# Kernel tuning notes

Hardware: AMD Instinct MI355X
Metric: run time of the kernel (lower is better)

The kernel has to match this reference:

```python
import jax, jax.numpy as jnp
import numpy as np
from jax import lax

# Model config (matches init_kwargs)
D = 256          # input_size
DO = 256         # output_size
H = 512          # hidden_size
E = 8            # num_experts
NB = 4           # num_bands
R = 8            # lora_rank
ALPHA = 16.0     # lora_alpha
CAP_F = 1.25     # capacity_factor
F = 64           # dct_freq_features
N = 65536        # num tokens
CAP = int(CAP_F * N / E)  # 10240 tokens per expert (expert-choice capacity)


def setup_inputs() -> dict:
    key = jax.random.key(0)
    ks = jax.random.split(key, 14)
    s = 0.02
    return {
        "x": jax.random.normal(ks[0], (N, D), jnp.float32),
        "band": jax.random.randint(ks[1], (N,), 0, NB, jnp.int32),
        "W_dct": jax.random.normal(ks[2], (D, F), jnp.float32) * s,
        "W_gate": jax.random.normal(ks[3], (D + F, E), jnp.float32) * s,
        "W1": jax.random.normal(ks[4], (E, D + 1, H), jnp.float32) * s,
        "b1": jnp.zeros((E, H), jnp.float32),
        "A1": jax.random.normal(ks[5], (E, NB, D + 1, R), jnp.float32) * s,
        "B1": jax.random.normal(ks[6], (E, NB, R, H), jnp.float32) * s,
        "W2": jax.random.normal(ks[7], (E, H, DO), jnp.float32) * s,
        "b2": jnp.zeros((E, DO), jnp.float32),
        "A2": jax.random.normal(ks[8], (E, NB, H, R), jnp.float32) * s,
        "B2": jax.random.normal(ks[9], (E, NB, R, DO), jnp.float32) * s,
    }


def reference(x, band, W_dct, W_gate, W1, b1, A1, B1, W2, b2, A2, B2):
    scale = ALPHA / R
    # 1) Frequency-aware gating: concat spatial + (linear) DCT-like features.
    freq = x @ W_dct                                   # [N,F]
    logits = jnp.concatenate([x, freq], -1) @ W_gate   # [N,E]
    # Expert-choice: softmax over the TOKEN axis, each expert picks top-CAP tokens.
    scores = jax.nn.softmax(logits, axis=0)            # [N,E]
    g, idx = lax.top_k(scores.T, CAP)                  # [E,CAP] weights / token ids
    # 2) Dispatch: gather tokens (band scalar appended -> input_size+1 features).
    band_f = band.astype(x.dtype)[:, None] / NB        # [N,1]
    x_full = jnp.concatenate([x, band_f], -1)          # [N,D+1]
    xe = x_full[idx]                                   # [E,CAP,D+1]
    oh = jax.nn.one_hot(band[idx], NB, dtype=x.dtype)  # [E,CAP,NB]
    ohn = jnp.transpose(oh, (0, 2, 1))[..., None]      # [E,NB,CAP,1]
    # 3) Per-expert shared MLP with per-band LoRA adapters (layer 1).
    h = jnp.einsum('ecd,edh->ech', xe, W1) + b1[:, None, :]
    u = jnp.einsum('ecd,endr->encr', xe, A1) * ohn     # band-select low-rank code
    h = h + scale * jnp.einsum('encr,enrh->ech', u, B1)
    h = jax.nn.gelu(h)
    # Layer 2.
    o = jnp.einsum('ech,eho->eco', h, W2) + b2[:, None, :]
    v = jnp.einsum('ech,enhr->encr', h, A2) * ohn
    o = o + scale * jnp.einsum('encr,enro->eco', v, B2)
    # 4) Combine: scatter-add gate-weighted expert outputs (unselected tokens -> 0).
    y = jnp.zeros((N, DO), x.dtype)
    y = y.at[idx.reshape(-1)].add((g[..., None] * o).reshape(-1, DO))
    return y
```

## Files before the change

kernel.cpp:

```cpp
#include <hip/hip_runtime.h>
#include <hip/hip_bf16.h>
#include <math.h>

#define NTOK 65536
#define DIN 256
#define DOUT 256
#define HID 512
#define NEXP 8
#define NBAND 4
#define RANK 8
#define CAP 10240
#define NTILE 64
#define TILES_PER_E (CAP / NTILE)

#define W1CAT_PER_E (34 * 9 * 512)
#define B1CAT_OFF   (NEXP * W1CAT_PER_E)
#define B1CAT_PER_E (32 * 512)
#define W2CAT_OFF   (B1CAT_OFF + NEXP * B1CAT_PER_E)
#define W2CAT_PER_E (18 * 16 * 512)
#define B2CAT_OFF   (W2CAT_OFF + NEXP * W2CAT_PER_E)
#define B2CAT_PER_E (16 * 512)
#define PK_TOTAL    (B2CAT_OFF + NEXP * B2CAT_PER_E)
#define PK_F32_OFF  1200000

typedef short s16x8 __attribute__((ext_vector_type(8)));
typedef float f32x4 __attribute__((ext_vector_type(4)));

__device__ __forceinline__ unsigned key_of(float f) {
    unsigned u = __float_as_uint(f);
    return (u & 0x80000000u) ? ~u : (u | 0x80000000u);
}
__device__ __forceinline__ float gelu_fast(float v) {
    const float c = 0.7978845608028654f;
    float z = c * (v + 0.044715f * v * v * v);
    float e = __expf(2.0f * z);
    return v * (1.0f - __builtin_amdgcn_rcpf(e + 1.0f));
}
__device__ __forceinline__ ushort f2bf(float f) {
    unsigned u = __float_as_uint(f);
    return (ushort)((u + 0x7FFFu + ((u >> 16) & 1u)) >> 16);
}

__global__ __launch_bounds__(256) void k_logits(const float* __restrict__ x,
                                                const float* __restrict__ Wdct,
                                                const float* __restrict__ Wgate,
                                                float* __restrict__ logitsT,
                                                float* __restrict__ partials,
                                                float* __restrict__ y) {
    __shared__ float wefft[8][257];
    __shared__ float pr[4][8];
    int tid = threadIdx.x, w = tid >> 6, lane = tid & 63;

    {
        int d = tid;
        float acc[8];
#pragma unroll
        for (int e = 0; e < 8; ++e) acc[e] = Wgate[d * 8 + e];
        for (int f = 0; f < 64; ++f) {
            float wv = Wdct[d * 64 + f];
#pragma unroll
            for (int e = 0; e < 8; ++e) acc[e] += wv * Wgate[(256 + f) * 8 + e];
        }
#pragma unroll
        for (int e = 0; e < 8; ++e) wefft[e][d] = acc[e];
    }

    {
        float4 z = {0.f, 0.f, 0.f, 0.f};
        float4* yp = (float4*)(y + (size_t)blockIdx.x * 64 * DOUT);
        for (int i = tid; i < 4096; i += 256) yp[i] = z;
    }
    __syncthreads();

    float wje[4][8];
#pragma unroll
    for (int j = 0; j < 4; ++j)
#pragma unroll
        for (int e = 0; e < 8; ++e) wje[j][e] = wefft[e][lane * 4 + j];

    int wid = blockIdx.x * 4 + w;
    int nbase = wid * 16;
    float es = 0.f;
    for (int t = 0; t < 16; ++t) {
        int n = nbase + t;
        float4 v = *(const float4*)(x + (size_t)n * DIN + lane * 4);
        float acc[8];
#pragma unroll
        for (int e = 0; e < 8; ++e) acc[e] = 0.f;
#pragma unroll
        for (int j = 0; j < 4; ++j) {
            float vj = (j == 0) ? v.x : (j == 1) ? v.y : (j == 2) ? v.z : v.w;
#pragma unroll
            for (int e = 0; e < 8; ++e) acc[e] += vj * wje[j][e];
        }
#pragma unroll
        for (int off = 1; off < 64; off <<= 1) {
#pragma unroll
            for (int e = 0; e < 8; ++e) acc[e] += __shfl_xor(acc[e], off);
        }
        float out = acc[0];
#pragma unroll
        for (int e = 1; e < 8; ++e) if (lane == e) out = acc[e];
        if (lane < 8) {
            logitsT[(size_t)lane * NTOK + n] = out;
            es += expf(out);
        }
    }
    if (lane < 8) pr[w][lane] = es;
    __syncthreads();
    if (tid < 8) partials[(size_t)tid * 1024 + blockIdx.x] =
        pr[0][tid] + pr[1][tid] + pr[2][tid] + pr[3][tid];
}

__global__ __launch_bounds__(1024) void k_misc(const float* __restrict__ logitsT,
                                               const float* __restrict__ partials,
                                               float* __restrict__ colsum,
                                               int* __restrict__ idxbuf,
                                               const float* __restrict__ W1,
                                               const float* __restrict__ A1,
                                               const float* __restrict__ B1,
                                               const float* __restrict__ W2,
                                               const float* __restrict__ A2,
                                               const float* __restrict__ B2,
                                               ushort* __restrict__ pk) {
    if (blockIdx.x >= 8) {
        int id = (blockIdx.x - 8) * 1024 + threadIdx.x;
        if (id >= PK_TOTAL) return;
        float val;
        if (id < B1CAT_OFF) {
            int e = id / W1CAT_PER_E, rem = id % W1CAT_PER_E;
            int t = rem / (9 * 512); rem %= 9 * 512;
            int s = rem / 512; int q = rem & 511;
            int l = q >> 3, j = q & 7;
            int k = s * 32 + ((l >> 4) << 3) + j;
            int col = t * 16 + (l & 15);
            if (k > 256) val = 0.f;
            else if (col < 512) val = W1[((size_t)e * 257 + k) * 512 + col];
            else {
                int cu = col - 512;
                val = A1[(((size_t)e * NBAND + (cu >> 3)) * 257 + k) * RANK + (cu & 7)];
            }
        } else if (id < W2CAT_OFF) {
            int id2 = id - B1CAT_OFF;
            int e = id2 / B1CAT_PER_E, rem = id2 % B1CAT_PER_E;
            int t = rem / 512; int q = rem & 511;
            int l = q >> 3, j = q & 7;
            int k32 = ((l >> 4) << 3) + j;
            int col = t * 16 + (l & 15);
            val = 2.0f * B1[(((size_t)e * NBAND + (k32 >> 3)) * RANK + (k32 & 7)) * 512 + col];
        } else if (id < B2CAT_OFF) {
            int id2 = id - W2CAT_OFF;
            int e = id2 / W2CAT_PER_E, rem = id2 % W2CAT_PER_E;
            int t = rem / (16 * 512); rem %= 16 * 512;
            int s = rem / 512; int q = rem & 511;
            int l = q >> 3, j = q & 7;
            int k = s * 32 + ((l >> 4) << 3) + j;
            int col = t * 16 + (l & 15);
            if (col < 256) val = W2[((size_t)e * 512 + k) * 256 + col];
            else {
                int cv = col - 256;
                val = A2[(((size_t)e * NBAND + (cv >> 3)) * 512 + k) * RANK + (cv & 7)];
            }
        } else {
            int id2 = id - B2CAT_OFF;
            int e = id2 / B2CAT_PER_E, rem = id2 % B2CAT_PER_E;
            int t = rem / 512; int q = rem & 511;
            int l = q >> 3, j = q & 7;
            int k32 = ((l >> 4) << 3) + j;
            int col = t * 16 + (l & 15);
            val = 2.0f * B2[(((size_t)e * NBAND + (k32 >> 3)) * RANK + (k32 & 7)) * 256 + col];
        }
        pk[id] = f2bf(val);
        return;
    }
    __shared__ unsigned subh[16][257];
    __shared__ unsigned bins[256];
    __shared__ float ssum[16];
    __shared__ unsigned sval[2];
    __shared__ unsigned scnt, stcnt;
    __shared__ int ties_l[2048];
    int e = blockIdx.x, tid = threadIdx.x, w = tid >> 6, lane = tid & 63;
    const float* lp = logitsT + (size_t)e * NTOK;

    {
        float s = partials[(size_t)e * 1024 + tid];
#pragma unroll
        for (int off = 32; off > 0; off >>= 1) s += __shfl_xor(s, off);
        if (lane == 0) ssum[w] = s;
        __syncthreads();
        if (tid == 0) {
            float t = 0.f;
#pragma unroll
            for (int i = 0; i < 16; ++i) t += ssum[i];
            colsum[e] = t;
        }
    }

    unsigned pref = 0, rem = CAP;
    for (int p = 0; p < 4; ++p) {
        int shift = 24 - 8 * p;
        for (int i = tid; i < 16 * 257; i += 1024) ((unsigned*)subh)[i] = 0;
        __syncthreads();
        for (int it = 0; it < 64; ++it) {
            int n = it * 1024 + tid;
            unsigned k = key_of(lp[n]);
            bool ok = (p == 0) || ((k >> (shift + 8)) == pref);
            if (ok) atomicAdd(&subh[w][(k >> shift) & 255u], 1u);
        }
        __syncthreads();
        if (tid < 256) {
            unsigned c = 0;
#pragma unroll
            for (int ww = 0; ww < 16; ++ww) c += subh[ww][tid];
            bins[tid] = c;
        }
        __syncthreads();
        for (int off = 1; off < 256; off <<= 1) {
            unsigned add = (tid < 256 && tid + off < 256) ? bins[tid + off] : 0u;
            __syncthreads();
            if (tid < 256) bins[tid] += add;
            __syncthreads();
        }
        if (tid < 256) {
            unsigned snext = (tid == 255) ? 0u : bins[tid + 1];
            if (bins[tid] >= rem && snext < rem) {
                sval[0] = (pref << 8) | (unsigned)tid;
                sval[1] = rem - snext;
            }
        }
        __syncthreads();
        pref = sval[0];
        rem = sval[1];
        __syncthreads();
    }

    if (tid == 0) { scnt = 0; stcnt = 0; }
    __syncthreads();
    unsigned T = pref;
    for (int it = 0; it < 64; ++it) {
        int n = it * 1024 + tid;
        unsigned k = key_of(lp[n]);
        if (k > T) {
            unsigned pos = atomicAdd(&scnt, 1u);
            idxbuf[e * CAP + pos] = n;
        } else if (k == T) {
            unsigned tp = atomicAdd(&stcnt, 1u);
            if (tp < 2048) ties_l[tp] = n;
        }
    }
    __syncthreads();
    int m = (int)stcnt, r = (int)rem, base = CAP - r;
    if (m == r) {
        for (int i = tid; i < m; i += 1024) idxbuf[e * CAP + base + i] = ties_l[i];
    } else {
        for (int i = tid; i < m; i += 1024) {
            int my = ties_l[i];
            int rank = 0;
            for (int j = 0; j < m; ++j) rank += (ties_l[j] < my);
            if (rank < r) idxbuf[e * CAP + base + rank] = my;
        }
    }
}

__global__ __launch_bounds__(256, 2) void k_expert(
    const float* __restrict__ x, const int* __restrict__ band,
    const float* __restrict__ b1, const float* __restrict__ b2,
    const ushort* __restrict__ pk,
    const float* __restrict__ logitsT,
    const float* __restrict__ colsum, const int* __restrict__ idxbuf,
    float* __restrict__ y) {
    __shared__ ushort bW1[9216];
    __shared__ ushort bW2[9216];
    __shared__ ushort sc[4][640];
    __shared__ int s_tok[4][16];
    __shared__ int s_band[4][16];
    __shared__ float s_g[4][16];

    int tid = threadIdx.x, w = tid >> 6, lane = tid & 63;
    int bid = blockIdx.x;
    int e = bid & 7;
    int tile = bid >> 3;

    if (lane < 16) {
        int n = idxbuf[e * CAP + tile * NTILE + w * 16 + lane];
        s_tok[w][lane] = n;
        s_band[w][lane] = band[n];
        s_g[w][lane] = expf(logitsT[(size_t)e * NTOK + n]) / colsum[e];
    }

    int l15 = lane & 15, lg = lane >> 4;
    ushort* scw = &sc[w][0];

    s16x8 a1[9];
    {
        int mytok = s_tok[w][l15];
        const float* xrow = x + (size_t)mytok * DIN;
        int kg = lg << 3;
#pragma unroll
        for (int s = 0; s < 8; ++s) {
            float4 p = *(const float4*)&xrow[s * 32 + kg];
            float4 q = *(const float4*)&xrow[s * 32 + kg + 4];
            s16x8 a;
            a[0] = (short)f2bf(p.x); a[1] = (short)f2bf(p.y);
            a[2] = (short)f2bf(p.z); a[3] = (short)f2bf(p.w);
            a[4] = (short)f2bf(q.x); a[5] = (short)f2bf(q.y);
            a[6] = (short)f2bf(q.z); a[7] = (short)f2bf(q.w);
            a1[s] = a;
        }
        s16x8 a = (s16x8)(short)0;
        if (lane < 16) a[0] = (short)f2bf((float)s_band[w][l15] * 0.25f);
        a1[8] = a;
    }

    const ushort* w1base = pk + (size_t)e * W1CAT_PER_E;
    const ushort* b1base = pk + B1CAT_OFF + (size_t)e * B1CAT_PER_E;
    const ushort* w2base = pk + W2CAT_OFF + (size_t)e * W2CAT_PER_E;
    const ushort* b2base = pk + B2CAT_OFF + (size_t)e * B2CAT_PER_E;

    s16x8 stg[9];
    if (w < 2) {
        const ushort* s0 = w2base + (size_t)(w * 9) * 16 * 512 + lane * 8;
#pragma unroll
        for (int i = 0; i < 9; ++i)
            stg[i] = *(const s16x8*)(s0 + (size_t)i * 16 * 512);
    } else {
        const ushort* s0 = w1base + (size_t)(w - 2) * 9 * 512 + lane * 8;
#pragma unroll
        for (int i = 0; i < 9; ++i)
            stg[i] = *(const s16x8*)(s0 + i * 512);
    }

    s16x8 ufrag;
    {
#pragma unroll
        for (int t = 32; t <= 33; ++t) {
            f32x4 acc = {0.f, 0.f, 0.f, 0.f};
#pragma unroll
            for (int s = 0; s < 9; ++s) {
                s16x8 b = *(const s16x8*)(w1base + ((size_t)t * 9 + s) * 512 + lane * 8);
                acc = __builtin_amdgcn_mfma_f32_16x16x32_bf16(a1[s], b, acc, 0, 0, 0);
            }
            int colbase = (t - 32) * 16 + l15;
#pragma unroll
            for (int r = 0; r < 4; ++r) {
                int row = lg * 4 + r;
                float v = ((colbase >> 3) == s_band[w][row]) ? acc[r] : 0.f;
                scw[row * 40 + colbase] = f2bf(v);
            }
        }
        ufrag = *(const s16x8*)&scw[l15 * 40 + lg * 8];
    }

    f32x4 oacc[16];
#pragma unroll
    for (int t2 = 0; t2 < 16; ++t2) {
        float bv = b2[(size_t)e * DOUT + t2 * 16 + l15];
        oacc[t2] = (f32x4){bv, bv, bv, bv};
    }
    f32x4 vacc[2];
    vacc[0] = (f32x4){0.f, 0.f, 0.f, 0.f};
    vacc[1] = (f32x4){0.f, 0.f, 0.f, 0.f};

    if (w < 2) {
#pragma unroll
        for (int i = 0; i < 9; ++i)
            *(s16x8*)(&bW2[(w * 9 + i) * 512] + lane * 8) = stg[i];
    } else {
#pragma unroll
        for (int i = 0; i < 9; ++i)
            *(s16x8*)(&bW1[((w - 2) * 9 + i) * 512] + lane * 8) = stg[i];
    }
    __syncthreads();

#pragma unroll 1
    for (int p = 0; p < 16; ++p) {
        s16x8 st2[9];
        if (p < 15) {
            int p1 = p + 1;
            if (w < 2) {
                const ushort* s0 = w2base + ((size_t)(w * 9) * 16 + p1) * 512 + lane * 8;
#pragma unroll
                for (int i = 0; i < 9; ++i)
                    st2[i] = *(const s16x8*)(s0 + (size_t)i * 16 * 512);
            } else {
                int t = p1 * 2 + (w - 2);
                const ushort* s0 = w1base + (size_t)t * 9 * 512 + lane * 8;
#pragma unroll
                for (int i = 0; i < 9; ++i)
                    st2[i] = *(const s16x8*)(s0 + i * 512);
            }
        }
#pragma unroll
        for (int half = 0; half < 2; ++half) {
            int t = p * 2 + half;
            float bv = b1[(size_t)e * HID + t * 16 + l15];
            f32x4 acc = {bv, bv, bv, bv};
#pragma unroll
            for (int s = 0; s < 9; ++s) {
                s16x8 b = *(const s16x8*)(&bW1[(half * 9 + s) * 512] + lane * 8);
                acc = __builtin_amdgcn_mfma_f32_16x16x32_bf16(a1[s], b, acc, 0, 0, 0);
            }
            {
                s16x8 b = *(const s16x8*)(b1base + (size_t)t * 512 + lane * 8);
                acc = __builtin_amdgcn_mfma_f32_16x16x32_bf16(ufrag, b, acc, 0, 0, 0);
            }
#pragma unroll
            for (int r = 0; r < 4; ++r) {
                int row = lg * 4 + r;
                scw[row * 40 + half * 16 + l15] = f2bf(gelu_fast(acc[r]));
            }
        }
        s16x8 hfrag = *(const s16x8*)&scw[l15 * 40 + lg * 8];
#pragma unroll
        for (int t2 = 0; t2 < 16; ++t2) {
            s16x8 b = *(const s16x8*)(&bW2[t2 * 512] + lane * 8);
            oacc[t2] = __builtin_amdgcn_mfma_f32_16x16x32_bf16(hfrag, b, oacc[t2], 0, 0, 0);
        }
#pragma unroll
        for (int i = 0; i < 2; ++i) {
            s16x8 b = *(const s16x8*)(&bW2[(16 + i) * 512] + lane * 8);
            vacc[i] = __builtin_amdgcn_mfma_f32_16x16x32_bf16(hfrag, b, vacc[i], 0, 0, 0);
        }
        if (p < 15) {
            __syncthreads();
            if (w < 2) {
#pragma unroll
                for (int i = 0; i < 9; ++i)
                    *(s16x8*)(&bW2[(w * 9 + i) * 512] + lane * 8) = st2[i];
            } else {
#pragma unroll
                for (int i = 0; i < 9; ++i)
                    *(s16x8*)(&bW1[((w - 2) * 9 + i) * 512] + lane * 8) = st2[i];
            }
            __syncthreads();
        }
    }

    s16x8 vfrag;
    {
#pragma unroll
        for (int i = 0; i < 2; ++i) {
            int colbase = i * 16 + l15;
#pragma unroll
            for (int r = 0; r < 4; ++r) {
                int row = lg * 4 + r;
                float v = ((colbase >> 3) == s_band[w][row]) ? vacc[i][r] : 0.f;
                scw[row * 40 + colbase] = f2bf(v);
            }
        }
        vfrag = *(const s16x8*)&scw[l15 * 40 + lg * 8];
    }

    float g4[4];
    int tok4[4];
#pragma unroll
    for (int r = 0; r < 4; ++r) {
        int row = lg * 4 + r;
        g4[r] = s_g[w][row];
        tok4[r] = s_tok[w][row];
    }
#pragma unroll
    for (int t2 = 0; t2 < 16; ++t2) {
        s16x8 b = *(const s16x8*)(b2base + (size_t)t2 * 512 + lane * 8);
        f32x4 acc = __builtin_amdgcn_mfma_f32_16x16x32_bf16(vfrag, b, oacc[t2], 0, 0, 0);
        int col = t2 * 16 + l15;
#pragma unroll
        for (int r = 0; r < 4; ++r) {
            atomicAdd(&y[(size_t)tok4[r] * DOUT + col], g4[r] * acc[r]);
        }
    }
}

extern "C" void kernel_launch(void* const* d_in, const int* in_sizes, int n_in,
                              void* d_out, int out_size, void* d_ws, size_t ws_size,
                              hipStream_t stream) {
    const float* x = (const float*)d_in[0];
    const int* band = (const int*)d_in[1];
    const float* Wdct = (const float*)d_in[2];
    const float* Wgate = (const float*)d_in[3];
    const float* W1 = (const float*)d_in[4];
    const float* b1 = (const float*)d_in[5];
    const float* A1 = (const float*)d_in[6];
    const float* B1 = (const float*)d_in[7];
    const float* W2 = (const float*)d_in[8];
    const float* b2 = (const float*)d_in[9];
    const float* A2 = (const float*)d_in[10];
    const float* B2 = (const float*)d_in[11];
    float* y = (float*)d_out;

    float* ws = (float*)d_ws;
    float* logitsT = ws;
    float* partials = ws + 524288;
    float* colsum = ws + 532480;
    int* idxbuf = (int*)(ws + 532488);
    ushort* pk = (ushort*)(ws + PK_F32_OFF);

    k_logits<<<1024, 256, 0, stream>>>(x, Wdct, Wgate, logitsT, partials, y);
    k_misc<<<8 + PK_TOTAL / 1024, 1024, 0, stream>>>(logitsT, partials, colsum,
                                                     idxbuf, W1, A1, B1, W2, A2,
                                                     B2, pk);
    k_expert<<<NEXP * TILES_PER_E, 256, 0, stream>>>(x, band, b1, b2, pk,
                                                     logitsT, colsum, idxbuf, y);
}
```

Measured before the change: 287.7 us.

## Build 16-bit key histogram in logits kernel to replace 4-pass radix top-k select

The logits kernel now atomically bins the top 16 bits of each logit's sortable key into a per-expert global histogram. The selection kernel uses that histogram in one prefix-scan pass to find the threshold bin, replacing four radix-histogram passes over all 65536 logits per expert. Ties within the threshold bin are written to a global buffer and ranked by full key then index, which can be quadratic if that bin is large. The expert kernel's launch bound also moves from 2 to 3 blocks per SIMD, which may cause register spilling.

```diff
diff --git a/kernel.cpp b/kernel.cpp
--- a/kernel.cpp
+++ b/kernel.cpp
@@ -12,6 +12,7 @@
 #define CAP 10240
 #define NTILE 64
 #define TILES_PER_E (CAP / NTILE)
+#define TIEMAX 7000
 
 #define W1CAT_PER_E (34 * 9 * 512)
 #define B1CAT_OFF   (NEXP * W1CAT_PER_E)
@@ -46,7 +47,8 @@
                                                 const float* __restrict__ Wgate,
                                                 float* __restrict__ logitsT,
                                                 float* __restrict__ partials,
-                                                float* __restrict__ y) {
+                                                float* __restrict__ y,
+                                                unsigned* __restrict__ hist16) {
     __shared__ float wefft[8][257];
     __shared__ float pr[4][8];
     int tid = threadIdx.x, w = tid >> 6, lane = tid & 63;
@@ -104,6 +106,7 @@
         if (lane < 8) {
             logitsT[(size_t)lane * NTOK + n] = out;
             es += expf(out);
+            atomicAdd(&hist16[((size_t)lane << 16) + (key_of(out) >> 16)], 1u);
         }
     }
     if (lane < 8) pr[w][lane] = es;
@@ -116,6 +119,8 @@
                                                const float* __restrict__ partials,
                                                float* __restrict__ colsum,
                                                int* __restrict__ idxbuf,
+                                               const unsigned* __restrict__ hist16,
+                                               int* __restrict__ tbuf,
                                                const float* __restrict__ W1,
                                                const float* __restrict__ A1,
                                                const float* __restrict__ B1,
@@ -173,14 +178,14 @@
         pk[id] = f2bf(val);
         return;
     }
-    __shared__ unsigned subh[16][257];
-    __shared__ unsigned bins[256];
+    __shared__ unsigned chunk[1024];
     __shared__ float ssum[16];
     __shared__ unsigned sval[2];
     __shared__ unsigned scnt, stcnt;
-    __shared__ int ties_l[2048];
     int e = blockIdx.x, tid = threadIdx.x, w = tid >> 6, lane = tid & 63;
     const float* lp = logitsT + (size_t)e * NTOK;
+    const unsigned* h = hist16 + ((size_t)e << 16);
+    int* tb = tbuf + (size_t)e * TIEMAX;
 
     {
         float s = partials[(size_t)e * 1024 + tid];
@@ -195,74 +200,64 @@
             colsum[e] = t;
         }
     }
-
-    unsigned pref = 0, rem = CAP;
-    for (int p = 0; p < 4; ++p) {
-        int shift = 24 - 8 * p;
-        for (int i = tid; i < 16 * 257; i += 1024) ((unsigned*)subh)[i] = 0;
+    if (tid == 0) { scnt = 0; stcnt = 0; }
+
+    {
+        unsigned csum = 0;
+        for (int i = 0; i < 64; ++i) csum += h[tid * 64 + i];
+        chunk[tid] = csum;
         __syncthreads();
-        for (int it = 0; it < 64; ++it) {
-            int n = it * 1024 + tid;
-            unsigned k = key_of(lp[n]);
-            bool ok = (p == 0) || ((k >> (shift + 8)) == pref);
-            if (ok) atomicAdd(&subh[w][(k >> shift) & 255u], 1u);
+        for (int off = 1; off < 1024; off <<= 1) {
+            unsigned add = (tid + off < 1024) ? chunk[tid + off] : 0u;
+            __syncthreads();
+            chunk[tid] += add;
+            __syncthreads();
+        }
+        unsigned above = (tid == 1023) ? 0u : chunk[tid + 1];
+        unsigned s = above;
+        for (int b = 63; b >= 0; --b) {
+            unsigned prev = s;
+            s += h[tid * 64 + b];
+            if (s >= (unsigned)CAP && prev < (unsigned)CAP) {
+                sval[0] = (unsigned)(tid * 64 + b);
+                sval[1] = (unsigned)CAP - prev;
+            }
         }
         __syncthreads();
-        if (tid < 256) {
-            unsigned c = 0;
-#pragma unroll
-            for (int ww = 0; ww < 16; ++ww) c += subh[ww][tid];
-            bins[tid] = c;
-        }
-        __syncthreads();
-        for (int off = 1; off < 256; off <<= 1) {
-            unsigned add = (tid < 256 && tid + off < 256) ? bins[tid + off] : 0u;
-            __syncthreads();
-            if (tid < 256) bins[tid] += add;
-            __syncthreads();
-        }
-        if (tid < 256) {
-            unsigned snext = (tid == 255) ? 0u : bins[tid + 1];
-            if (bins[tid] >= rem && snext < rem) {
-                sval[0] = (pref << 8) | (unsigned)tid;
-                sval[1] = rem - snext;
-            }
-        }
-        __syncthreads();
-        pref = sval[0];
-        rem = sval[1];
-        __syncthreads();
-    }
-
-    if (tid == 0) { scnt = 0; stcnt = 0; }
-    __syncthreads();
-    unsigned T = pref;
+    }
+    unsigned B = sval[0], rem = sval[1];
+
     for (int it = 0; it < 64; ++it) {
         int n = it * 1024 + tid;
-        unsigned k = key_of(lp[n]);
-        if (k > T) {
+        unsigned k16 = key_of(lp[n]) >> 16;
+        if (k16 > B) {
             unsigned pos = atomicAdd(&scnt, 1u);
             idxbuf[e * CAP + pos] = n;
-        } else if (k == T) {
+        } else if (k16 == B) {
             unsigned tp = atomicAdd(&stcnt, 1u);
-            if (tp < 2048) ties_l[tp] = n;
+            if (tp < TIEMAX) tb[tp] = n;
         }
     }
     __syncthreads();
-    int m = (int)stcnt, r = (int)rem, base = CAP - r;
+    int m = (int)min(stcnt, (unsigned)TIEMAX), r = (int)rem, base = CAP - r;
     if (m == r) {
-        for (int i = tid; i < m; i += 1024) idxbuf[e * CAP + base + i] = ties_l[i];
+        for (int i = tid; i < m; i += 1024) idxbuf[e * CAP + base + i] = tb[i];
     } else {
         for (int i = tid; i < m; i += 1024) {
-            int my = ties_l[i];
+            int my = tb[i];
+            unsigned km = key_of(lp[my]);
             int rank = 0;
-            for (int j = 0; j < m; ++j) rank += (ties_l[j] < my);
+            for (int j = 0; j < m; ++j) {
+                int oj = tb[j];
+                unsigned kj = key_of(lp[oj]);
+                rank += (kj > km) || (kj == km && oj < my);
+            }
             if (rank < r) idxbuf[e * CAP + base + rank] = my;
         }
     }
 }
 
-__global__ __launch_bounds__(256, 2) void k_expert(
+__global__ __launch_bounds__(256, 3) void k_expert(
     const float* __restrict__ x, const int* __restrict__ band,
     const float* __restrict__ b1, const float* __restrict__ b2,
     const ushort* __restrict__ pk,
@@ -493,12 +488,16 @@
     float* partials = ws + 524288;
     float* colsum = ws + 532480;
     int* idxbuf = (int*)(ws + 532488);
+    unsigned* hist16 = (unsigned*)(ws + 614408);
+    int* tbuf = (int*)(ws + 1138696);
     ushort* pk = (ushort*)(ws + PK_F32_OFF);
 
-    k_logits<<<1024, 256, 0, stream>>>(x, Wdct, Wgate, logitsT, partials, y);
+    hipMemsetAsync(hist16, 0, 524288 * sizeof(unsigned), stream);
+
+    k_logits<<<1024, 256, 0, stream>>>(x, Wdct, Wgate, logitsT, partials, y, hist16);
     k_misc<<<8 + PK_TOTAL / 1024, 1024, 0, stream>>>(logitsT, partials, colsum,
-                                                     idxbuf, W1, A1, B1, W2, A2,
-                                                     B2, pk);
+                                                     idxbuf, hist16, tbuf,
+                                                     W1, A1, B1, W2, A2, B2, pk);
     k_expert<<<NEXP * TILES_PER_E, 256, 0, stream>>>(x, band, b1, b2, pk,
                                                      logitsT, colsum, idxbuf, y);
 }
```

Measured after the change: 368.2 us. 28.0% more time.
